# Kernel tuning notes

Measured on AMD Instinct MI355X. Metric: run time of the kernel, lower is better.

The kernel has to match this reference:

```python
import math
import jax, jax.numpy as jnp
import numpy as np

D = 512
H = 8
N_COLS = 2048            # n + 1
D_COL = math.ceil(2 * math.log2(N_COLS))  # 22
B = 8
N_KEEP = 768
T = N_KEEP + 1


def setup_inputs() -> dict:
    key = jax.random.key(0)
    ks = jax.random.split(key, 12)
    inp = {
        "x_head": jax.random.normal(ks[0], (B, T, D), jnp.float32),
        "x_tail": jax.random.normal(ks[1], (B, T, D), jnp.float32),
        "ids_keep": jax.random.randint(ks[2], (B, N_KEEP), 0, N_COLS - 1),
        # W_tail is tied to W_head (sym_weight=True)
        "W_head_w": jax.random.normal(ks[3], (D, D), jnp.float32) * (1.0 / math.sqrt(D)),
        "W_head_b": jnp.zeros((D,), jnp.float32),
        "W_v_w": jax.random.normal(ks[4], (D, D), jnp.float32) * (1.0 / math.sqrt(D)),
        "W_v_b": jnp.zeros((D,), jnp.float32),
        "W_out_w": jax.random.normal(ks[5], (D, D), jnp.float32) * (1.0 / math.sqrt(D)),
        "W_out_b": jnp.zeros((D,), jnp.float32),
        "rel_emb": jnp.ones((H, D // H), jnp.float32),
        "col_head": jax.random.normal(ks[6], (H, N_COLS, D_COL), jnp.float32),
        "col_tail": jax.random.normal(ks[7], (H, N_COLS, D_COL), jnp.float32),
        "bias": jnp.zeros((1,), jnp.float32),
    }
    return inp


def _split_heads(x, n_heads):
    b, t, d = x.shape
    return x.reshape(b, t, n_heads, d // n_heads).transpose(0, 2, 1, 3)  # [B,H,T,dh]


def _gather_cols(col_emb, ids_keep):
    """col_emb: [H, N_COLS, d_col] (L2-normalized). Gather kept feature rows per
    batch element and re-prepend the CLS/readout row -> [B, H, 1+n_keep, d_col]."""
    cls = col_emb[:, :1, :]                       # [H,1,dc]
    feats = col_emb[:, 1:, :]                     # [H,N_COLS-1,dc]
    kept = jnp.take(feats, ids_keep, axis=1)      # [H,B,nk,dc]
    kept = kept.transpose(1, 0, 2, 3)             # [B,H,nk,dc]
    cls_b = jnp.broadcast_to(cls[None], (kept.shape[0],) + cls.shape)  # [B,H,1,dc]
    return jnp.concatenate([cls_b, kept], axis=2)


def reference(x_head, x_tail, ids_keep, W_head_w, W_head_b, W_v_w, W_v_b,
              W_out_w, W_out_b, rel_emb, col_head, col_tail, bias):
    n_heads = rel_emb.shape[0]
    d_head = rel_emb.shape[1]
    b, t, _ = x_head.shape

    # Projections (W_tail tied to W_head)
    f_head = x_head @ W_head_w.T + W_head_b
    f_tail = x_tail @ W_head_w.T + W_head_b
    f_v = x_tail @ W_v_w.T + W_v_b

    fh = _split_heads(f_head, n_heads)  # [B,H,T,dh]
    ft = _split_heads(f_tail, n_heads)
    fv = _split_heads(f_v, n_heads)

    # relation-weighted score: f_head @ diag(rel_emb) @ f_tail^T / sqrt(dh)
    weight_score = jnp.einsum('bhqd,bhkd->bhqk', fh * rel_emb[None, :, None, :], ft)
    weight_score = weight_score / math.sqrt(d_head)

    # Normalized topology embeddings + masked-token gather
    ch = col_head / jnp.linalg.norm(col_head, axis=-1, keepdims=True)
    ct = col_tail / jnp.linalg.norm(col_tail, axis=-1, keepdims=True)
    ch = _gather_cols(ch, ids_keep)  # [B,H,T,dc]
    ct = _gather_cols(ct, ids_keep)
    top_score = jnp.einsum('bhqd,bhkd->bhqk', ch, ct)  # [B,H,T,T]

    # Topology -> straight-through binary adjacency
    adj_probs = jax.nn.sigmoid(top_score + bias[0])
    nsi_mask = 1.0 - jnp.eye(t, dtype=adj_probs.dtype)          # no self-interaction
    adj_probs = adj_probs * nsi_mask
    readout_mask = jnp.ones((t,), adj_probs.dtype).at[0].set(0.0)  # prune edges to readout
    adj_probs = adj_probs * readout_mask
    adj = (adj_probs > 0.5).astype(adj_probs.dtype) - jax.lax.stop_gradient(adj_probs) + adj_probs

    adj_mask = (1.0 - adj) * -10000.0
    fr_graph = jax.nn.softmax(weight_score + adj_mask, axis=-1)

    x = jnp.einsum('bhqk,bhkd->bhqd', fr_graph, fv)
    x = x.transpose(0, 2, 1, 3).reshape(b, t, n_heads * fv.shape[-1])
    x = x @ W_out_w.T + W_out_b
    return (x, jax.lax.stop_gradient(fr_graph))
```

## Files before the change

### kernel.cpp

```cpp
#include <hip/hip_runtime.h>

#define D_     512
#define H_     8
#define NCOLS_ 2048
#define DCOL_  22
#define B_     8
#define NKEEP_ 768
#define T_     769
#define BT_    (B_*T_)
#define BH_    (B_*H_)

typedef __attribute__((ext_vector_type(8))) short bf16x8;
typedef __attribute__((ext_vector_type(4))) float f32x4;

__device__ __forceinline__ ushort f2bf(float f) {
    unsigned u = __float_as_uint(f);
    unsigned r = u + 0x7fffu + ((u >> 16) & 1u);
    return (ushort)(r >> 16);
}

__global__ __launch_bounds__(256) void cast_bf16(
    const float* __restrict__ src, ushort* __restrict__ dst, int n4)
{
    int i = blockIdx.x * 256 + threadIdx.x;
    if (i >= n4) return;
    float4 v = ((const float4*)src)[i];
    ushort4 o;
    o.x = f2bf(v.x); o.y = f2bf(v.y); o.z = f2bf(v.z); o.w = f2bf(v.w);
    ((ushort4*)dst)[i] = o;
}

__global__ __launch_bounds__(256) void gemm_mfma(
    const ushort* __restrict__ A, const ushort* __restrict__ W,
    const float* __restrict__ bias, const float* __restrict__ rel,
    ushort* __restrict__ outb, float* __restrict__ outf,
    const int M, const int mode)
{
    __shared__ __align__(16) ushort As[128*40];
    __shared__ __align__(16) ushort Bs[128*40];
    const int t    = threadIdx.x;
    const int lane = t & 63;
    const int wv   = t >> 6;
    const int wr   = wv >> 1, wc = wv & 1;
    const int m16  = lane & 15, q4 = lane >> 4;
    const int m0   = blockIdx.y * 128;
    const int n0   = blockIdx.x * 128;
    const int sr   = t >> 1;
    const int sh   = t & 1;

    f32x4 acc[4][4] = {};
    for (int k0 = 0; k0 < 512; k0 += 32) {
        {
            int row = m0 + sr;
            bf16x8 z = {};
            bf16x8 v0 = z, v1 = z;
            if (row < M) {
                const bf16x8* gp = (const bf16x8*)(A + (size_t)row*512 + k0 + sh*16);
                v0 = gp[0]; v1 = gp[1];
            }
            *(bf16x8*)&As[sr*40 + sh*16]     = v0;
            *(bf16x8*)&As[sr*40 + sh*16 + 8] = v1;
            const bf16x8* wp = (const bf16x8*)(W + (size_t)(n0 + sr)*512 + k0 + sh*16);
            *(bf16x8*)&Bs[sr*40 + sh*16]     = wp[0];
            *(bf16x8*)&Bs[sr*40 + sh*16 + 8] = wp[1];
        }
        __syncthreads();
        bf16x8 a[4], b[4];
        #pragma unroll
        for (int i = 0; i < 4; ++i)
            a[i] = *(const bf16x8*)&As[(wr*64 + i*16 + m16)*40 + q4*8];
        #pragma unroll
        for (int j = 0; j < 4; ++j)
            b[j] = *(const bf16x8*)&Bs[(wc*64 + j*16 + m16)*40 + q4*8];
        #pragma unroll
        for (int i = 0; i < 4; ++i)
            #pragma unroll
            for (int j = 0; j < 4; ++j)
                acc[i][j] = __builtin_amdgcn_mfma_f32_16x16x32_bf16(a[i], b[j], acc[i][j], 0, 0, 0);
        __syncthreads();
    }

    #pragma unroll
    for (int j = 0; j < 4; ++j) {
        const int n = n0 + wc*64 + j*16 + m16;
        const float bn = bias[n];
        const float sc = (mode == 0) ? rel[n] * 0.125f : 1.0f;
        const int h = n >> 6, dh = n & 63;
        #pragma unroll
        for (int i = 0; i < 4; ++i) {
            #pragma unroll
            for (int r = 0; r < 4; ++r) {
                int m = m0 + wr*64 + i*16 + q4*4 + r;
                if (m >= M) continue;
                float v = acc[i][j][r] + bn;
                if (mode == 3) {
                    outf[(size_t)m*512 + n] = v;
                } else {
                    if (mode == 0) v *= sc;
                    int bb = m / T_, tt = m - bb*T_;
                    outb[(((size_t)bb*H_ + h)*T_ + tt)*64 + dh] = f2bf(v);
                }
            }
        }
    }
}

__global__ void gather_norm(
    const float* __restrict__ col_head, const float* __restrict__ col_tail,
    const int* __restrict__ ids, float* __restrict__ chg, float* __restrict__ ctg)
{
    int r = blockIdx.x * blockDim.x + threadIdx.x;
    const int total = BH_ * T_;
    if (r >= 2*total) return;
    const bool tail = (r >= total);
    int rr = tail ? r - total : r;
    int bh = rr / T_;
    int q  = rr - bh*T_;
    int b  = bh >> 3, h = bh & 7;
    int src = (q == 0) ? 0 : (1 + ids[b*NKEEP_ + q - 1]);
    const float* cp = (tail ? col_tail : col_head) + ((size_t)h*NCOLS_ + src)*DCOL_;
    float v[DCOL_];
    float ss = 0.f;
    #pragma unroll
    for (int j = 0; j < DCOL_; ++j) { v[j] = cp[j]; ss += v[j]*v[j]; }
    float inv = 1.0f / sqrtf(ss);
    float* op = (tail ? ctg : chg) + (size_t)rr*DCOL_;
    #pragma unroll
    for (int j = 0; j < DCOL_; ++j) op[j] = v[j]*inv;
}

__global__ __launch_bounds__(256) void score_mfma(
    const ushort* __restrict__ fhb, const ushort* __restrict__ ftb,
    const float* __restrict__ chg, const float* __restrict__ ctg,
    const float* __restrict__ biasp, float* __restrict__ fr)
{
    __shared__ __align__(16) char smem[128*72*2*2];
    float*  Gq = (float*)smem;
    float*  Gk = Gq + 22*132;
    ushort* Qs = (ushort*)smem;
    ushort* Ks = Qs + 128*72;

    const int bh = blockIdx.z;
    const int q0 = blockIdx.y * 128;
    const int k0 = blockIdx.x * 128;
    const int t    = threadIdx.x;
    const int lane = t & 63;
    const int wv   = t >> 6;
    const int wr   = wv >> 1, wc = wv & 1;
    const int m16  = lane & 15, q4 = lane >> 4;

    {
        if (t < 128) {
            int q = q0 + t;
            const float* p = chg + ((size_t)bh*T_ + q)*DCOL_;
            #pragma unroll 2
            for (int d = 0; d < DCOL_; ++d)
                Gq[d*132 + t] = (q < T_) ? p[d] : 0.f;
        } else {
            int r = t - 128;
            int k = k0 + r;
            const float* p = ctg + ((size_t)bh*T_ + k)*DCOL_;
            #pragma unroll 2
            for (int d = 0; d < DCOL_; ++d)
                Gk[d*132 + r] = (k < T_) ? p[d] : 0.f;
        }
    }
    __syncthreads();

    unsigned long long km = 0ull;
    {
        float ga[4][4][4] = {};
        #pragma unroll 2
        for (int d = 0; d < DCOL_; ++d) {
            float4 aq[4];
            float  bk[4];
            #pragma unroll
            for (int i = 0; i < 4; ++i)
                aq[i] = *(const float4*)&Gq[d*132 + wr*64 + i*16 + q4*4];
            #pragma unroll
            for (int j = 0; j < 4; ++j)
                bk[j] = Gk[d*132 + wc*64 + j*16 + m16];
            #pragma unroll
            for (int i = 0; i < 4; ++i) {
                float av[4] = {aq[i].x, aq[i].y, aq[i].z, aq[i].w};
                #pragma unroll
                for (int r = 0; r < 4; ++r)
                    #pragma unroll
                    for (int j = 0; j < 4; ++j)
                        ga[i][r][j] += av[r] * bk[j];
            }
        }
        const float bias0 = biasp[0];
        #pragma unroll
        for (int i = 0; i < 4; ++i)
            #pragma unroll
            for (int r = 0; r < 4; ++r)
                #pragma unroll
                for (int j = 0; j < 4; ++j)
                    if (ga[i][r][j] + bias0 > 0.f)
                        km |= 1ull << (i*16 + r*4 + j);
    }
    __syncthreads();

    {
        const int sr = t >> 1, sh = t & 1;
        int q = q0 + sr, k = k0 + sr;
        bf16x8 z = {};
        const bf16x8* qp = (const bf16x8*)(fhb + ((size_t)bh*T_ + q)*64 + sh*32);
        const bf16x8* kp = (const bf16x8*)(ftb + ((size_t)bh*T_ + k)*64 + sh*32);
        #pragma unroll
        for (int e = 0; e < 4; ++e) {
            *(bf16x8*)&Qs[sr*72 + sh*32 + e*8] = (q < T_) ? qp[e] : z;
            *(bf16x8*)&Ks[sr*72 + sh*32 + e*8] = (k < T_) ? kp[e] : z;
        }
    }
    __syncthreads();

    f32x4 acc[4][4] = {};
    #pragma unroll
    for (int c = 0; c < 2; ++c) {
        bf16x8 a[4], b[4];
        #pragma unroll
        for (int i = 0; i < 4; ++i)
            a[i] = *(const bf16x8*)&Qs[(wr*64 + i*16 + m16)*72 + c*32 + q4*8];
        #pragma unroll
        for (int j = 0; j < 4; ++j)
            b[j] = *(const bf16x8*)&Ks[(wc*64 + j*16 + m16)*72 + c*32 + q4*8];
        #pragma unroll
        for (int i = 0; i < 4; ++i)
            #pragma unroll
            for (int j = 0; j < 4; ++j)
                acc[i][j] = __builtin_amdgcn_mfma_f32_16x16x32_bf16(a[i], b[j], acc[i][j], 0, 0, 0);
    }

    #pragma unroll
    for (int i = 0; i < 4; ++i) {
        #pragma unroll
        for (int j = 0; j < 4; ++j) {
            const int k = k0 + wc*64 + j*16 + m16;
            #pragma unroll
            for (int r = 0; r < 4; ++r) {
                int q = q0 + wr*64 + i*16 + q4*4 + r;
                if (q >= T_ || k >= T_) continue;
                bool kp = ((km >> (i*16 + r*4 + j)) & 1ull) && (q != k) && (k != 0);
                fr[((size_t)bh*T_ + q)*T_ + k] = acc[i][j][r] + (kp ? 0.f : -10000.f);
            }
        }
    }
}

__global__ __launch_bounds__(256) void softmax_kernel(float* __restrict__ fr)
{
    __shared__ float red[4];
    const int t = threadIdx.x;
    float* p = fr + (size_t)blockIdx.x * T_;
    float v[4];
    float m = -3.4e38f;
    #pragma unroll
    for (int i = 0; i < 4; ++i) {
        int idx = t + i*256;
        v[i] = (idx < T_) ? p[idx] : -3.4e38f;
        m = fmaxf(m, v[i]);
    }
    #pragma unroll
    for (int off = 32; off > 0; off >>= 1) m = fmaxf(m, __shfl_xor(m, off, 64));
    if ((t & 63) == 0) red[t >> 6] = m;
    __syncthreads();
    m = fmaxf(fmaxf(red[0], red[1]), fmaxf(red[2], red[3]));
    __syncthreads();
    float e[4]; float s = 0.f;
    #pragma unroll
    for (int i = 0; i < 4; ++i) {
        int idx = t + i*256;
        e[i] = (idx < T_) ? expf(v[i] - m) : 0.f;
        s += e[i];
    }
    #pragma unroll
    for (int off = 32; off > 0; off >>= 1) s += __shfl_xor(s, off, 64);
    if ((t & 63) == 0) red[t >> 6] = s;
    __syncthreads();
    s = red[0] + red[1] + red[2] + red[3];
    float inv = 1.0f / s;
    #pragma unroll
    for (int i = 0; i < 4; ++i) {
        int idx = t + i*256;
        if (idx < T_) p[idx] = e[i] * inv;
    }
}

__global__ __launch_bounds__(256) void pv_mfma(
    const float* __restrict__ fr, const ushort* __restrict__ fvb,
    ushort* __restrict__ x1b)
{
    __shared__ __align__(16) ushort Ps[128*40];
    __shared__ __align__(16) ushort Vs[64*40];
    const int bh = blockIdx.y;
    const int b = bh >> 3, h = bh & 7;
    const int q0 = blockIdx.x * 128;
    const int t    = threadIdx.x;
    const int lane = t & 63;
    const int wv   = t >> 6;
    const int m16  = lane & 15, q4 = lane >> 4;

    f32x4 acc[2][4] = {};
    for (int kk0 = 0; kk0 < 800; kk0 += 32) {
        {
            const int sr = t >> 1, sh = t & 1;
            int q = q0 + sr;
            const float* p = fr + ((size_t)bh*T_ + ((q < T_) ? q : 0))*T_ + kk0 + sh*16;
            ushort tmp[16];
            if (q < T_ && kk0 + sh*16 + 15 < T_) {
                #pragma unroll
                for (int e = 0; e < 4; ++e) {
                    float4 v = *(const float4*)(p + e*4);
                    tmp[e*4+0] = f2bf(v.x); tmp[e*4+1] = f2bf(v.y);
                    tmp[e*4+2] = f2bf(v.z); tmp[e*4+3] = f2bf(v.w);
                }
            } else {
                #pragma unroll
                for (int e = 0; e < 16; ++e) {
                    int k = kk0 + sh*16 + e;
                    tmp[e] = (q < T_ && k < T_) ? f2bf(p[e]) : (ushort)0;
                }
            }
            *(bf16x8*)&Ps[sr*40 + sh*16]     = *(bf16x8*)&tmp[0];
            *(bf16x8*)&Ps[sr*40 + sh*16 + 8] = *(bf16x8*)&tmp[8];
        }
        {
            const int dg = t >> 5;
            const int k  = t & 31;
            int kg = kk0 + k;
            ushort vv[8];
            if (kg < T_) {
                const bf16x8 v = *(const bf16x8*)(fvb + ((size_t)bh*T_ + kg)*64 + dg*8);
                #pragma unroll
                for (int e = 0; e < 8; ++e) vv[e] = ((ushort)(v[e]));
            } else {
                #pragma unroll
                for (int e = 0; e < 8; ++e) vv[e] = 0;
            }
            #pragma unroll
            for (int e = 0; e < 8; ++e)
                Vs[(dg*8 + e)*40 + k] = vv[e];
        }
        __syncthreads();
        bf16x8 a[2], bb[4];
        #pragma unroll
        for (int i = 0; i < 2; ++i)
            a[i] = *(const bf16x8*)&Ps[(wv*32 + i*16 + m16)*40 + q4*8];
        #pragma unroll
        for (int j = 0; j < 4; ++j)
            bb[j] = *(const bf16x8*)&Vs[(j*16 + m16)*40 + q4*8];
        #pragma unroll
        for (int i = 0; i < 2; ++i)
            #pragma unroll
            for (int j = 0; j < 4; ++j)
                acc[i][j] = __builtin_amdgcn_mfma_f32_16x16x32_bf16(a[i], bb[j], acc[i][j], 0, 0, 0);
        __syncthreads();
    }

    #pragma unroll
    for (int i = 0; i < 2; ++i) {
        #pragma unroll
        for (int j = 0; j < 4; ++j) {
            const int d = j*16 + m16;
            #pragma unroll
            for (int r = 0; r < 4; ++r) {
                int q = q0 + wv*32 + i*16 + q4*4 + r;
                if (q >= T_) continue;
                x1b[((size_t)b*T_ + q)*512 + h*64 + d] = f2bf(acc[i][j][r]);
            }
        }
    }
}

extern "C" void kernel_launch(void* const* d_in, const int* in_sizes, int n_in,
                              void* d_out, int out_size, void* d_ws, size_t ws_size,
                              hipStream_t stream)
{
    (void)in_sizes; (void)n_in; (void)out_size; (void)ws_size;
    const float* x_head   = (const float*)d_in[0];
    const float* x_tail   = (const float*)d_in[1];
    const int*   ids      = (const int*)  d_in[2];
    const float* W_head_w = (const float*)d_in[3];
    const float* W_head_b = (const float*)d_in[4];
    const float* W_v_w    = (const float*)d_in[5];
    const float* W_v_b    = (const float*)d_in[6];
    const float* W_out_w  = (const float*)d_in[7];
    const float* W_out_b  = (const float*)d_in[8];
    const float* rel      = (const float*)d_in[9];
    const float* col_h    = (const float*)d_in[10];
    const float* col_t    = (const float*)d_in[11];
    const float* biasp    = (const float*)d_in[12];

    const size_t F   = (size_t)BH_*T_*64;
    const size_t WSZ = 512*512;
    const size_t C22 = (size_t)BH_*T_*DCOL_;

    char* ws = (char*)d_ws;
    ushort* fhb = (ushort*)ws;            ws += F*2;
    ushort* ftb = (ushort*)ws;            ws += F*2;
    ushort* fvb = (ushort*)ws;            ws += F*2;
    ushort* xhb = (ushort*)ws;            ws += F*2;
    ushort* xtb = (ushort*)ws;            ws += F*2;
    ushort* whb = (ushort*)ws;            ws += WSZ*2;
    ushort* wvb = (ushort*)ws;            ws += WSZ*2;
    ushort* wob = (ushort*)ws;            ws += WSZ*2;
    float*  chg = (float*)ws;             ws += C22*4;
    float*  ctg = (float*)ws;             ws += C22*4;
    ushort* x1b = xhb;

    float* xout = (float*)d_out;
    float* fr   = xout + (size_t)BT_*D_;

    dim3 blk(256, 1, 1);

    cast_bf16<<<(int)((F/4 + 255)/256),   blk, 0, stream>>>(x_head,   xhb, (int)(F/4));
    cast_bf16<<<(int)((F/4 + 255)/256),   blk, 0, stream>>>(x_tail,   xtb, (int)(F/4));
    cast_bf16<<<(int)((WSZ/4 + 255)/256), blk, 0, stream>>>(W_head_w, whb, (int)(WSZ/4));
    cast_bf16<<<(int)((WSZ/4 + 255)/256), blk, 0, stream>>>(W_v_w,    wvb, (int)(WSZ/4));
    cast_bf16<<<(int)((WSZ/4 + 255)/256), blk, 0, stream>>>(W_out_w,  wob, (int)(WSZ/4));

    dim3 gProj(4, 49, 1);
    gemm_mfma<<<gProj, blk, 0, stream>>>(xhb, whb, W_head_b, rel, fhb, nullptr, BT_, 0);
    gemm_mfma<<<gProj, blk, 0, stream>>>(xtb, whb, W_head_b, rel, ftb, nullptr, BT_, 1);
    gemm_mfma<<<gProj, blk, 0, stream>>>(xtb, wvb, W_v_b,    rel, fvb, nullptr, BT_, 1);

    int gatherThreads = 2 * BH_ * T_;
    gather_norm<<<(gatherThreads + 255)/256, blk, 0, stream>>>(col_h, col_t, ids, chg, ctg);

    dim3 gScore(7, 7, BH_);
    score_mfma<<<gScore, blk, 0, stream>>>(fhb, ftb, chg, ctg, biasp, fr);

    softmax_kernel<<<BH_*T_, blk, 0, stream>>>(fr);

    dim3 gPV(7, BH_, 1);
    pv_mfma<<<gPV, blk, 0, stream>>>(fr, fvb, x1b);

    gemm_mfma<<<gProj, blk, 0, stream>>>(x1b, wob, W_out_b, rel, nullptr, xout, BT_, 3);
}
```

Baseline: 479.3 us.

## Fuse score, softmax and PV into one flash-style kernel; fold casts into projections

Replaces the separate score, softmax and PV kernels with a single fused attention kernel. It computes the topology mask and the QK scores, exponentiates without max subtraction, accumulates P·V in MFMA, and writes unnormalized bf16 probabilities that a follow-up kernel rescales into fp32. The fp32→bf16 casts move into the projection GEMM loads, and the three input projections are batched into one launch. This removes most of the fp32 fr round trips and several launches. In exchange it lowers fr precision, and fully masked rows get zeros instead of the reference's uniform distribution.

```diff
diff --git a/kernel.cpp b/kernel.cpp
--- a/kernel.cpp
+++ b/kernel.cpp
@@ -18,26 +18,31 @@
     unsigned r = u + 0x7fffu + ((u >> 16) & 1u);
     return (ushort)(r >> 16);
 }
-
-__global__ __launch_bounds__(256) void cast_bf16(
-    const float* __restrict__ src, ushort* __restrict__ dst, int n4)
-{
-    int i = blockIdx.x * 256 + threadIdx.x;
-    if (i >= n4) return;
-    float4 v = ((const float4*)src)[i];
-    ushort4 o;
-    o.x = f2bf(v.x); o.y = f2bf(v.y); o.z = f2bf(v.z); o.w = f2bf(v.w);
-    ((ushort4*)dst)[i] = o;
-}
-
-__global__ __launch_bounds__(256) void gemm_mfma(
-    const ushort* __restrict__ A, const ushort* __restrict__ W,
-    const float* __restrict__ bias, const float* __restrict__ rel,
-    ushort* __restrict__ outb, float* __restrict__ outf,
-    const int M, const int mode)
+__device__ __forceinline__ float bf2f(ushort u) {
+    return __uint_as_float(((unsigned)u) << 16);
+}
+
+__global__ __launch_bounds__(256) void proj_mfma(
+    const float* __restrict__ xh, const float* __restrict__ xt,
+    const ushort* __restrict__ x1b,
+    const float* __restrict__ Wh, const float* __restrict__ Wv,
+    const float* __restrict__ Wo,
+    const float* __restrict__ bh_, const float* __restrict__ bv_,
+    const float* __restrict__ bo_, const float* __restrict__ rel,
+    ushort* __restrict__ fhb, ushort* __restrict__ ftb,
+    ushort* __restrict__ fvb, float* __restrict__ xout, const int jobParam)
 {
     __shared__ __align__(16) ushort As[128*40];
     __shared__ __align__(16) ushort Bs[128*40];
+    const int job = (jobParam < 0) ? (int)blockIdx.z : jobParam;
+    const float* A32 = nullptr; const ushort* A16 = nullptr;
+    const float* W; const float* bias;
+    ushort* outb = nullptr; float* outf = nullptr; int mode;
+    if (job == 0)      { A32 = xh; W = Wh; bias = bh_; outb = fhb; mode = 0; }
+    else if (job == 1) { A32 = xt; W = Wh; bias = bh_; outb = ftb; mode = 1; }
+    else if (job == 2) { A32 = xt; W = Wv; bias = bv_; outb = fvb; mode = 1; }
+    else               { A16 = x1b; W = Wo; bias = bo_; outf = xout; mode = 3; }
+
     const int t    = threadIdx.x;
     const int lane = t & 63;
     const int wv   = t >> 6;
@@ -45,24 +50,45 @@
     const int m16  = lane & 15, q4 = lane >> 4;
     const int m0   = blockIdx.y * 128;
     const int n0   = blockIdx.x * 128;
-    const int sr   = t >> 1;
-    const int sh   = t & 1;
 
     f32x4 acc[4][4] = {};
     for (int k0 = 0; k0 < 512; k0 += 32) {
         {
-            int row = m0 + sr;
-            bf16x8 z = {};
-            bf16x8 v0 = z, v1 = z;
-            if (row < M) {
-                const bf16x8* gp = (const bf16x8*)(A + (size_t)row*512 + k0 + sh*16);
-                v0 = gp[0]; v1 = gp[1];
-            }
-            *(bf16x8*)&As[sr*40 + sh*16]     = v0;
-            *(bf16x8*)&As[sr*40 + sh*16 + 8] = v1;
-            const bf16x8* wp = (const bf16x8*)(W + (size_t)(n0 + sr)*512 + k0 + sh*16);
-            *(bf16x8*)&Bs[sr*40 + sh*16]     = wp[0];
-            *(bf16x8*)&Bs[sr*40 + sh*16 + 8] = wp[1];
+            const int sr = t >> 1, sh = t & 1;
+            const int row = m0 + sr;
+            ushort ta[16];
+            if (A16) {
+                bf16x8 z = {}; bf16x8 v0 = z, v1 = z;
+                if (row < BT_) {
+                    const bf16x8* gp = (const bf16x8*)(A16 + (size_t)row*512 + k0 + sh*16);
+                    v0 = gp[0]; v1 = gp[1];
+                }
+                *(bf16x8*)&ta[0] = v0; *(bf16x8*)&ta[8] = v1;
+            } else {
+                #pragma unroll
+                for (int e = 0; e < 16; ++e) ta[e] = 0;
+                if (row < BT_) {
+                    const float* ap = A32 + (size_t)row*512 + k0 + sh*16;
+                    #pragma unroll
+                    for (int e = 0; e < 4; ++e) {
+                        float4 f = *(const float4*)(ap + e*4);
+                        ta[e*4+0]=f2bf(f.x); ta[e*4+1]=f2bf(f.y);
+                        ta[e*4+2]=f2bf(f.z); ta[e*4+3]=f2bf(f.w);
+                    }
+                }
+            }
+            *(bf16x8*)&As[sr*40 + sh*16]     = *(bf16x8*)&ta[0];
+            *(bf16x8*)&As[sr*40 + sh*16 + 8] = *(bf16x8*)&ta[8];
+            const float* wp = W + (size_t)(n0 + sr)*512 + k0 + sh*16;
+            ushort tw[16];
+            #pragma unroll
+            for (int e = 0; e < 4; ++e) {
+                float4 f = *(const float4*)(wp + e*4);
+                tw[e*4+0]=f2bf(f.x); tw[e*4+1]=f2bf(f.y);
+                tw[e*4+2]=f2bf(f.z); tw[e*4+3]=f2bf(f.w);
+            }
+            *(bf16x8*)&Bs[sr*40 + sh*16]     = *(bf16x8*)&tw[0];
+            *(bf16x8*)&Bs[sr*40 + sh*16 + 8] = *(bf16x8*)&tw[8];
         }
         __syncthreads();
         bf16x8 a[4], b[4];
@@ -91,7 +117,7 @@
             #pragma unroll
             for (int r = 0; r < 4; ++r) {
                 int m = m0 + wr*64 + i*16 + q4*4 + r;
-                if (m >= M) continue;
+                if (m >= BT_) continue;
                 float v = acc[i][j][r] + bn;
                 if (mode == 3) {
                     outf[(size_t)m*512 + n] = v;
@@ -129,249 +155,205 @@
     for (int j = 0; j < DCOL_; ++j) op[j] = v[j]*inv;
 }
 
-__global__ __launch_bounds__(256) void score_mfma(
+__global__ __launch_bounds__(256) void fused_attn(
     const ushort* __restrict__ fhb, const ushort* __restrict__ ftb,
-    const float* __restrict__ chg, const float* __restrict__ ctg,
-    const float* __restrict__ biasp, float* __restrict__ fr)
+    const ushort* __restrict__ fvb, const float* __restrict__ chg,
+    const float* __restrict__ ctg, const float* __restrict__ biasp,
+    float* __restrict__ fr, ushort* __restrict__ x1b, float* __restrict__ invA)
 {
-    __shared__ __align__(16) char smem[128*72*2*2];
-    float*  Gq = (float*)smem;
-    float*  Gk = Gq + 22*132;
-    ushort* Qs = (ushort*)smem;
-    ushort* Ks = Qs + 128*72;
-
-    const int bh = blockIdx.z;
-    const int q0 = blockIdx.y * 128;
-    const int k0 = blockIdx.x * 128;
+    __shared__ __align__(16) ushort Qs[64*72];
+    __shared__ __align__(16) ushort Ks[64*72];
+    __shared__ __align__(16) ushort Vs[64*72];
+    __shared__ __align__(16) ushort Et[64*72];
+    __shared__ __align__(16) float  Gq[DCOL_*68];
+    __shared__ __align__(16) float  Gk[DCOL_*68];
+    __shared__ float sumP[4*64];
+    __shared__ float inv_s[64];
+
+    const int bh = blockIdx.y;
+    const int q0 = blockIdx.x * 64;
     const int t    = threadIdx.x;
-    const int lane = t & 63;
-    const int wv   = t >> 6;
-    const int wr   = wv >> 1, wc = wv & 1;
+    const int lane = t & 63, w = t >> 6;
     const int m16  = lane & 15, q4 = lane >> 4;
+    const float bias0 = biasp[0];
 
     {
-        if (t < 128) {
-            int q = q0 + t;
-            const float* p = chg + ((size_t)bh*T_ + q)*DCOL_;
+        int qr = t >> 2, qc = min(q0 + qr, T_-1);
+        const ushort* qp = fhb + ((size_t)bh*T_ + qc)*64 + (t&3)*16;
+        *(bf16x8*)&Qs[qr*72 + (t&3)*16]     = *(const bf16x8*)qp;
+        *(bf16x8*)&Qs[qr*72 + (t&3)*16 + 8] = *(const bf16x8*)(qp + 8);
+    }
+    for (int idx = t; idx < 64*DCOL_; idx += 256) {
+        int r = idx / DCOL_, d = idx - r*DCOL_;
+        int qc = min(q0 + r, T_-1);
+        Gq[d*68 + r] = chg[((size_t)bh*T_ + qc)*DCOL_ + d];
+    }
+
+    float psum[4][4] = {};
+    f32x4 Oacc[4] = {};
+
+    for (int kt = 0; kt < 13; ++kt) {
+        const int k0g = kt*64;
+        __syncthreads();
+        {
+            int kr = t >> 2, kc = min(k0g + kr, T_-1);
+            const ushort* kp = ftb + ((size_t)bh*T_ + kc)*64 + (t&3)*16;
+            *(bf16x8*)&Ks[kr*72 + (t&3)*16]     = *(const bf16x8*)kp;
+            *(bf16x8*)&Ks[kr*72 + (t&3)*16 + 8] = *(const bf16x8*)(kp + 8);
+            const ushort* vp = fvb + ((size_t)bh*T_ + kc)*64 + (t&3)*16;
+            bf16x8 v0 = *(const bf16x8*)vp, v1 = *(const bf16x8*)(vp + 8);
+            int dbase = (t&3)*16;
+            #pragma unroll
+            for (int e = 0; e < 8; ++e) Vs[(dbase+e)*72 + kr]   = (ushort)v0[e];
+            #pragma unroll
+            for (int e = 0; e < 8; ++e) Vs[(dbase+8+e)*72 + kr] = (ushort)v1[e];
+        }
+        for (int idx = t; idx < 64*DCOL_; idx += 256) {
+            int r = idx / DCOL_, d = idx - r*DCOL_;
+            int kc = min(k0g + r, T_-1);
+            Gk[d*68 + r] = ctg[((size_t)bh*T_ + kc)*DCOL_ + d];
+        }
+        __syncthreads();
+
+        const int kL = w*16 + m16;
+        const int kg = k0g + kL;
+        unsigned kmask = 0;
+        {
+            float ga[4][4] = {};
             #pragma unroll 2
-            for (int d = 0; d < DCOL_; ++d)
-                Gq[d*132 + t] = (q < T_) ? p[d] : 0.f;
-        } else {
-            int r = t - 128;
-            int k = k0 + r;
-            const float* p = ctg + ((size_t)bh*T_ + k)*DCOL_;
-            #pragma unroll 2
-            for (int d = 0; d < DCOL_; ++d)
-                Gk[d*132 + r] = (k < T_) ? p[d] : 0.f;
-        }
+            for (int d = 0; d < DCOL_; ++d) {
+                float gk = Gk[d*68 + kL];
+                #pragma unroll
+                for (int i = 0; i < 4; ++i) {
+                    float4 a4 = *(const float4*)&Gq[d*68 + i*16 + q4*4];
+                    ga[i][0] += a4.x*gk; ga[i][1] += a4.y*gk;
+                    ga[i][2] += a4.z*gk; ga[i][3] += a4.w*gk;
+                }
+            }
+            const bool kok = (kg != 0) && (kg < T_);
+            #pragma unroll
+            for (int i = 0; i < 4; ++i)
+                #pragma unroll
+                for (int r = 0; r < 4; ++r) {
+                    int qg = q0 + i*16 + q4*4 + r;
+                    if (kok && (ga[i][r] + bias0 > 0.f) && (qg != kg))
+                        kmask |= 1u << (i*4 + r);
+                }
+        }
+
+        f32x4 Sacc[4] = {};
+        #pragma unroll
+        for (int step = 0; step < 2; ++step) {
+            bf16x8 b = *(const bf16x8*)&Ks[kL*72 + step*32 + q4*8];
+            #pragma unroll
+            for (int i = 0; i < 4; ++i) {
+                bf16x8 a = *(const bf16x8*)&Qs[(i*16 + m16)*72 + step*32 + q4*8];
+                Sacc[i] = __builtin_amdgcn_mfma_f32_16x16x32_bf16(a, b, Sacc[i], 0, 0, 0);
+            }
+        }
+
+        #pragma unroll
+        for (int i = 0; i < 4; ++i) {
+            #pragma unroll
+            for (int r = 0; r < 4; ++r) {
+                float e = ((kmask >> (i*4 + r)) & 1u) ? __expf(Sacc[i][r]) : 0.f;
+                psum[i][r] += e;
+                Et[(i*16 + q4*4 + r)*72 + kL] = f2bf(e);
+            }
+        }
+        __syncthreads();
+
+        #pragma unroll
+        for (int step = 0; step < 2; ++step) {
+            bf16x8 a = *(const bf16x8*)&Et[(w*16 + m16)*72 + step*32 + q4*8];
+            #pragma unroll
+            for (int j = 0; j < 4; ++j) {
+                bf16x8 b = *(const bf16x8*)&Vs[(j*16 + m16)*72 + step*32 + q4*8];
+                Oacc[j] = __builtin_amdgcn_mfma_f32_16x16x32_bf16(a, b, Oacc[j], 0, 0, 0);
+            }
+        }
+
+        {
+            const int c = t & 15;
+            #pragma unroll
+            for (int p = 0; p < 4; ++p) {
+                int row = p*16 + (t >> 4);
+                int qg = q0 + row;
+                if (qg >= T_) continue;
+                char* rowbase = (char*)(fr + ((size_t)bh*T_ + qg)*T_);
+                #pragma unroll
+                for (int e = 0; e < 2; ++e) {
+                    int dw = c + 16*e;
+                    int kk = k0g + dw*2;
+                    unsigned u = *(const unsigned*)&Et[row*72 + dw*2];
+                    if (kk + 1 < T_)      *(unsigned*)(rowbase + (size_t)kk*2) = u;
+                    else if (kk < T_)     *(ushort*)(rowbase + (size_t)kk*2) = (ushort)u;
+                }
+            }
+        }
+    }
+
+    #pragma unroll
+    for (int i = 0; i < 4; ++i)
+        #pragma unroll
+        for (int r = 0; r < 4; ++r) {
+            float v = psum[i][r];
+            v += __shfl_xor(v, 1, 64);
+            v += __shfl_xor(v, 2, 64);
+            v += __shfl_xor(v, 4, 64);
+            v += __shfl_xor(v, 8, 64);
+            psum[i][r] = v;
+        }
+    if (m16 == 0) {
+        #pragma unroll
+        for (int i = 0; i < 4; ++i)
+            #pragma unroll
+            for (int r = 0; r < 4; ++r)
+                sumP[w*64 + i*16 + q4*4 + r] = psum[i][r];
     }
     __syncthreads();
-
-    unsigned long long km = 0ull;
+    if (t < 64) {
+        float s = sumP[t] + sumP[64+t] + sumP[128+t] + sumP[192+t];
+        float iv = 1.0f / fmaxf(s, 1e-30f);
+        inv_s[t] = iv;
+        if (q0 + t < T_) invA[(size_t)bh*T_ + q0 + t] = iv;
+    }
+    __syncthreads();
+
     {
-        float ga[4][4][4] = {};
-        #pragma unroll 2
-        for (int d = 0; d < DCOL_; ++d) {
-            float4 aq[4];
-            float  bk[4];
-            #pragma unroll
-            for (int i = 0; i < 4; ++i)
-                aq[i] = *(const float4*)&Gq[d*132 + wr*64 + i*16 + q4*4];
-            #pragma unroll
-            for (int j = 0; j < 4; ++j)
-                bk[j] = Gk[d*132 + wc*64 + j*16 + m16];
-            #pragma unroll
-            for (int i = 0; i < 4; ++i) {
-                float av[4] = {aq[i].x, aq[i].y, aq[i].z, aq[i].w};
-                #pragma unroll
-                for (int r = 0; r < 4; ++r)
-                    #pragma unroll
-                    for (int j = 0; j < 4; ++j)
-                        ga[i][r][j] += av[r] * bk[j];
-            }
-        }
-        const float bias0 = biasp[0];
-        #pragma unroll
-        for (int i = 0; i < 4; ++i)
-            #pragma unroll
-            for (int r = 0; r < 4; ++r)
-                #pragma unroll
-                for (int j = 0; j < 4; ++j)
-                    if (ga[i][r][j] + bias0 > 0.f)
-                        km |= 1ull << (i*16 + r*4 + j);
-    }
+        const int b = bh >> 3, h = bh & 7;
+        #pragma unroll
+        for (int j = 0; j < 4; ++j) {
+            int d = j*16 + m16;
+            #pragma unroll
+            for (int r = 0; r < 4; ++r) {
+                int rr = w*16 + q4*4 + r;
+                int qg = q0 + rr;
+                if (qg < T_)
+                    x1b[((size_t)b*T_ + qg)*512 + h*64 + d] = f2bf(Oacc[j][r] * inv_s[rr]);
+            }
+        }
+    }
+}
+
+__global__ __launch_bounds__(256) void normalize_fr(
+    float* __restrict__ fr, const float* __restrict__ invA)
+{
+    const int row = blockIdx.x;
+    const int t = threadIdx.x;
+    float* rowp = fr + (size_t)row * T_;
+    const ushort* packed = (const ushort*)rowp;
+    const float iv = invA[row];
+    float v0 = bf2f(packed[t])       * iv;
+    float v1 = bf2f(packed[t + 256]) * iv;
+    float v2 = bf2f(packed[t + 512]) * iv;
+    float v3 = 0.f;
+    if (t == 0) v3 = bf2f(packed[768]) * iv;
     __syncthreads();
-
-    {
-        const int sr = t >> 1, sh = t & 1;
-        int q = q0 + sr, k = k0 + sr;
-        bf16x8 z = {};
-        const bf16x8* qp = (const bf16x8*)(fhb + ((size_t)bh*T_ + q)*64 + sh*32);
-        const bf16x8* kp = (const bf16x8*)(ftb + ((size_t)bh*T_ + k)*64 + sh*32);
-        #pragma unroll
-        for (int e = 0; e < 4; ++e) {
-            *(bf16x8*)&Qs[sr*72 + sh*32 + e*8] = (q < T_) ? qp[e] : z;
-            *(bf16x8*)&Ks[sr*72 + sh*32 + e*8] = (k < T_) ? kp[e] : z;
-        }
-    }
-    __syncthreads();
-
-    f32x4 acc[4][4] = {};
-    #pragma unroll
-    for (int c = 0; c < 2; ++c) {
-        bf16x8 a[4], b[4];
-        #pragma unroll
-        for (int i = 0; i < 4; ++i)
-            a[i] = *(const bf16x8*)&Qs[(wr*64 + i*16 + m16)*72 + c*32 + q4*8];
-        #pragma unroll
-        for (int j = 0; j < 4; ++j)
-            b[j] = *(const bf16x8*)&Ks[(wc*64 + j*16 + m16)*72 + c*32 + q4*8];
-        #pragma unroll
-        for (int i = 0; i < 4; ++i)
-            #pragma unroll
-            for (int j = 0; j < 4; ++j)
-                acc[i][j] = __builtin_amdgcn_mfma_f32_16x16x32_bf16(a[i], b[j], acc[i][j], 0, 0, 0);
-    }
-
-    #pragma unroll
-    for (int i = 0; i < 4; ++i) {
-        #pragma unroll
-        for (int j = 0; j < 4; ++j) {
-            const int k = k0 + wc*64 + j*16 + m16;
-            #pragma unroll
-            for (int r = 0; r < 4; ++r) {
-                int q = q0 + wr*64 + i*16 + q4*4 + r;
-                if (q >= T_ || k >= T_) continue;
-                bool kp = ((km >> (i*16 + r*4 + j)) & 1ull) && (q != k) && (k != 0);
-                fr[((size_t)bh*T_ + q)*T_ + k] = acc[i][j][r] + (kp ? 0.f : -10000.f);
-            }
-        }
-    }
-}
-
-__global__ __launch_bounds__(256) void softmax_kernel(float* __restrict__ fr)
-{
-    __shared__ float red[4];
-    const int t = threadIdx.x;
-    float* p = fr + (size_t)blockIdx.x * T_;
-    float v[4];
-    float m = -3.4e38f;
-    #pragma unroll
-    for (int i = 0; i < 4; ++i) {
-        int idx = t + i*256;
-        v[i] = (idx < T_) ? p[idx] : -3.4e38f;
-        m = fmaxf(m, v[i]);
-    }
-    #pragma unroll
-    for (int off = 32; off > 0; off >>= 1) m = fmaxf(m, __shfl_xor(m, off, 64));
-    if ((t & 63) == 0) red[t >> 6] = m;
-    __syncthreads();
-    m = fmaxf(fmaxf(red[0], red[1]), fmaxf(red[2], red[3]));
-    __syncthreads();
-    float e[4]; float s = 0.f;
-    #pragma unroll
-    for (int i = 0; i < 4; ++i) {
-        int idx = t + i*256;
-        e[i] = (idx < T_) ? expf(v[i] - m) : 0.f;
-        s += e[i];
-    }
-    #pragma unroll
-    for (int off = 32; off > 0; off >>= 1) s += __shfl_xor(s, off, 64);
-    if ((t & 63) == 0) red[t >> 6] = s;
-    __syncthreads();
-    s = red[0] + red[1] + red[2] + red[3];
-    float inv = 1.0f / s;
-    #pragma unroll
-    for (int i = 0; i < 4; ++i) {
-        int idx = t + i*256;
-        if (idx < T_) p[idx] = e[i] * inv;
-    }
-}
-
-__global__ __launch_bounds__(256) void pv_mfma(
-    const float* __restrict__ fr, const ushort* __restrict__ fvb,
-    ushort* __restrict__ x1b)
-{
-    __shared__ __align__(16) ushort Ps[128*40];
-    __shared__ __align__(16) ushort Vs[64*40];
-    const int bh = blockIdx.y;
-    const int b = bh >> 3, h = bh & 7;
-    const int q0 = blockIdx.x * 128;
-    const int t    = threadIdx.x;
-    const int lane = t & 63;
-    const int wv   = t >> 6;
-    const int m16  = lane & 15, q4 = lane >> 4;
-
-    f32x4 acc[2][4] = {};
-    for (int kk0 = 0; kk0 < 800; kk0 += 32) {
-        {
-            const int sr = t >> 1, sh = t & 1;
-            int q = q0 + sr;
-            const float* p = fr + ((size_t)bh*T_ + ((q < T_) ? q : 0))*T_ + kk0 + sh*16;
-            ushort tmp[16];
-            if (q < T_ && kk0 + sh*16 + 15 < T_) {
-                #pragma unroll
-                for (int e = 0; e < 4; ++e) {
-                    float4 v = *(const float4*)(p + e*4);
-                    tmp[e*4+0] = f2bf(v.x); tmp[e*4+1] = f2bf(v.y);
-                    tmp[e*4+2] = f2bf(v.z); tmp[e*4+3] = f2bf(v.w);
-                }
-            } else {
-                #pragma unroll
-                for (int e = 0; e < 16; ++e) {
-                    int k = kk0 + sh*16 + e;
-                    tmp[e] = (q < T_ && k < T_) ? f2bf(p[e]) : (ushort)0;
-                }
-            }
-            *(bf16x8*)&Ps[sr*40 + sh*16]     = *(bf16x8*)&tmp[0];
-            *(bf16x8*)&Ps[sr*40 + sh*16 + 8] = *(bf16x8*)&tmp[8];
-        }
-        {
-            const int dg = t >> 5;
-            const int k  = t & 31;
-            int kg = kk0 + k;
-            ushort vv[8];
-            if (kg < T_) {
-                const bf16x8 v = *(const bf16x8*)(fvb + ((size_t)bh*T_ + kg)*64 + dg*8);
-                #pragma unroll
-                for (int e = 0; e < 8; ++e) vv[e] = ((ushort)(v[e]));
-            } else {
-                #pragma unroll
-                for (int e = 0; e < 8; ++e) vv[e] = 0;
-            }
-            #pragma unroll
-            for (int e = 0; e < 8; ++e)
-                Vs[(dg*8 + e)*40 + k] = vv[e];
-        }
-        __syncthreads();
-        bf16x8 a[2], bb[4];
-        #pragma unroll
-        for (int i = 0; i < 2; ++i)
-            a[i] = *(const bf16x8*)&Ps[(wv*32 + i*16 + m16)*40 + q4*8];
-        #pragma unroll
-        for (int j = 0; j < 4; ++j)
-            bb[j] = *(const bf16x8*)&Vs[(j*16 + m16)*40 + q4*8];
-        #pragma unroll
-        for (int i = 0; i < 2; ++i)
-            #pragma unroll
-            for (int j = 0; j < 4; ++j)
-                acc[i][j] = __builtin_amdgcn_mfma_f32_16x16x32_bf16(a[i], bb[j], acc[i][j], 0, 0, 0);
-        __syncthreads();
-    }
-
-    #pragma unroll
-    for (int i = 0; i < 2; ++i) {
-        #pragma unroll
-        for (int j = 0; j < 4; ++j) {
-            const int d = j*16 + m16;
-            #pragma unroll
-            for (int r = 0; r < 4; ++r) {
-                int q = q0 + wv*32 + i*16 + q4*4 + r;
-                if (q >= T_) continue;
-                x1b[((size_t)b*T_ + q)*512 + h*64 + d] = f2bf(acc[i][j][r]);
-            }
-        }
-    }
+    rowp[t]       = v0;
+    rowp[t + 256] = v1;
+    rowp[t + 512] = v2;
+    if (t == 0) rowp[768] = v3;
 }
 
 extern "C" void kernel_launch(void* const* d_in, const int* in_sizes, int n_in,
@@ -394,48 +376,34 @@
     const float* biasp    = (const float*)d_in[12];
 
     const size_t F   = (size_t)BH_*T_*64;
-    const size_t WSZ = 512*512;
     const size_t C22 = (size_t)BH_*T_*DCOL_;
 
     char* ws = (char*)d_ws;
-    ushort* fhb = (ushort*)ws;            ws += F*2;
-    ushort* ftb = (ushort*)ws;            ws += F*2;
-    ushort* fvb = (ushort*)ws;            ws += F*2;
-    ushort* xhb = (ushort*)ws;            ws += F*2;
-    ushort* xtb = (ushort*)ws;            ws += F*2;
-    ushort* whb = (ushort*)ws;            ws += WSZ*2;
-    ushort* wvb = (ushort*)ws;            ws += WSZ*2;
-    ushort* wob = (ushort*)ws;            ws += WSZ*2;
-    float*  chg = (float*)ws;             ws += C22*4;
-    float*  ctg = (float*)ws;             ws += C22*4;
-    ushort* x1b = xhb;
+    ushort* fhb = (ushort*)ws;   ws += F*2;
+    ushort* ftb = (ushort*)ws;   ws += F*2;
+    ushort* fvb = (ushort*)ws;   ws += F*2;
+    ushort* x1b = (ushort*)ws;   ws += F*2;
+    float*  chg = (float*)ws;    ws += C22*4;
+    float*  ctg = (float*)ws;    ws += C22*4;
+    float*  invA = (float*)ws;   ws += (size_t)BH_*T_*4;
 
     float* xout = (float*)d_out;
     float* fr   = xout + (size_t)BT_*D_;
 
     dim3 blk(256, 1, 1);
 
-    cast_bf16<<<(int)((F/4 + 255)/256),   blk, 0, stream>>>(x_head,   xhb, (int)(F/4));
-    cast_bf16<<<(int)((F/4 + 255)/256),   blk, 0, stream>>>(x_tail,   xtb, (int)(F/4));
-    cast_bf16<<<(int)((WSZ/4 + 255)/256), blk, 0, stream>>>(W_head_w, whb, (int)(WSZ/4));
-    cast_bf16<<<(int)((WSZ/4 + 255)/256), blk, 0, stream>>>(W_v_w,    wvb, (int)(WSZ/4));
-    cast_bf16<<<(int)((WSZ/4 + 255)/256), blk, 0, stream>>>(W_out_w,  wob, (int)(WSZ/4));
-
-    dim3 gProj(4, 49, 1);
-    gemm_mfma<<<gProj, blk, 0, stream>>>(xhb, whb, W_head_b, rel, fhb, nullptr, BT_, 0);
-    gemm_mfma<<<gProj, blk, 0, stream>>>(xtb, whb, W_head_b, rel, ftb, nullptr, BT_, 1);
-    gemm_mfma<<<gProj, blk, 0, stream>>>(xtb, wvb, W_v_b,    rel, fvb, nullptr, BT_, 1);
-
-    int gatherThreads = 2 * BH_ * T_;
-    gather_norm<<<(gatherThreads + 255)/256, blk, 0, stream>>>(col_h, col_t, ids, chg, ctg);
-
-    dim3 gScore(7, 7, BH_);
-    score_mfma<<<gScore, blk, 0, stream>>>(fhb, ftb, chg, ctg, biasp, fr);
-
-    softmax_kernel<<<BH_*T_, blk, 0, stream>>>(fr);
-
-    dim3 gPV(7, BH_, 1);
-    pv_mfma<<<gPV, blk, 0, stream>>>(fr, fvb, x1b);
-
-    gemm_mfma<<<gProj, blk, 0, stream>>>(x1b, wob, W_out_b, rel, nullptr, xout, BT_, 3);
-}
+    gather_norm<<<(2*BH_*T_ + 255)/256, blk, 0, stream>>>(col_h, col_t, ids, chg, ctg);
+
+    proj_mfma<<<dim3(4, 49, 3), blk, 0, stream>>>(
+        x_head, x_tail, nullptr, W_head_w, W_v_w, W_out_w,
+        W_head_b, W_v_b, W_out_b, rel, fhb, ftb, fvb, nullptr, -1);
+
+    fused_attn<<<dim3(13, BH_), blk, 0, stream>>>(
+        fhb, ftb, fvb, chg, ctg, biasp, fr, x1b, invA);
+
+    normalize_fr<<<BH_*T_, blk, 0, stream>>>(fr, invA);
+
+    proj_mfma<<<dim3(4, 49, 1), blk, 0, stream>>>(
+        x_head, x_tail, x1b, W_head_w, W_v_w, W_out_w,
+        W_head_b, W_v_b, W_out_b, rel, fhb, ftb, fvb, xout, 3);
+}
```

Measured after the change: 453.0 us. 5.5% less time.
